# Kernel optimization log

Measured on AMD Instinct MI355X. Metric: run time of the kernel, lower is better.

The kernel has to match this reference:

```python
import jax, jax.numpy as jnp
import numpy as np

C = 512        # in_ch = n_heads * d_embed
NH = 8         # heads
DH = C // NH   # head dim = 64
G = 32         # groups
EPS_GN = 1e-6
EPS_LN = 1e-5


def group_norm(x, gamma, beta):
    # x: (B, C, H, W)
    B, Cc, H, W = x.shape
    xg = x.reshape(B, G, Cc // G, H, W)
    mu = xg.mean(axis=(2, 3, 4), keepdims=True)
    var = xg.var(axis=(2, 3, 4), keepdims=True)
    xg = (xg - mu) * jax.lax.rsqrt(var + EPS_GN)
    x = xg.reshape(B, Cc, H, W)
    return x * gamma[None, :, None, None] + beta[None, :, None, None]


def layer_norm(x, gamma, beta):
    mu = x.mean(axis=-1, keepdims=True)
    var = x.var(axis=-1, keepdims=True)
    return (x - mu) * jax.lax.rsqrt(var + EPS_LN) * gamma + beta


def mhsa(x, w_qkv, w_out, b_out):
    # x: (B, S, C); w_qkv: (C, 3C); w_out: (C, C)
    B, S, Cc = x.shape
    qkv = x @ w_qkv                                   # (B, S, 3C)
    q, k, v = jnp.split(qkv, 3, axis=-1)
    q = q.reshape(B, S, NH, DH).transpose(0, 2, 1, 3)  # (B, H, S, D)
    k = k.reshape(B, S, NH, DH).transpose(0, 2, 1, 3)
    v = v.reshape(B, S, NH, DH).transpose(0, 2, 1, 3)
    scores = jnp.einsum('bhsd,bhtd->bhst', q, k) / jnp.sqrt(jnp.float32(DH))
    attn = jax.nn.softmax(scores, axis=-1)
    o = jnp.einsum('bhst,bhtd->bhsd', attn, v)         # (B, H, S, D)
    o = o.transpose(0, 2, 1, 3).reshape(B, S, Cc)
    return o @ w_out + b_out


def conv1x1(x, w, b):
    # x: (B, C, H, W); w: (Cout, Cin)
    return jnp.einsum('oc,bchw->bohw', w, x) + b[None, :, None, None]


def reference(x, gn_g, gn_b, w_cin, b_cin,
              ln1_g, ln1_b, qkv1, out1_w, out1_b,
              ln2_g, ln2_b, qkv2, out2_w, out2_b,
              ln3_g, ln3_b, g1_w, g1_b, g2_w, g2_b,
              w_cout, b_cout):
    residue_long = x
    h = group_norm(x, gn_g, gn_b)
    h = conv1x1(h, w_cin, b_cin)
    B, Cc, H, W = h.shape
    h = h.reshape(B, Cc, H * W).transpose(0, 2, 1)     # (B, S, C)

    r = h
    h = mhsa(layer_norm(h, ln1_g, ln1_b), qkv1, out1_w, out1_b) + r
    r = h
    h = mhsa(layer_norm(h, ln2_g, ln2_b), qkv2, out2_w, out2_b) + r
    r = h
    g = layer_norm(h, ln3_g, ln3_b) @ g1_w + g1_b      # (B, S, 8C)
    val, gate = jnp.split(g, 2, axis=-1)
    h = (val * jax.nn.gelu(gate, approximate=False)) @ g2_w + g2_b
    h = h + r

    h = h.transpose(0, 2, 1).reshape(B, Cc, H, W)
    return conv1x1(h, w_cout, b_cout) + residue_long


def setup_inputs() -> dict:
    key = jax.random.key(0)
    ks = jax.random.split(key, 16)
    s = lambda n: 1.0 / np.sqrt(n)
    return {
        'x': jax.random.normal(ks[0], (8, C, 32, 32), jnp.float32),
        'gn_g': jnp.ones((C,), jnp.float32),
        'gn_b': jnp.zeros((C,), jnp.float32),
        'w_cin': jax.random.normal(ks[1], (C, C), jnp.float32) * s(C),
        'b_cin': jnp.zeros((C,), jnp.float32),
        'ln1_g': jnp.ones((C,), jnp.float32),
        'ln1_b': jnp.zeros((C,), jnp.float32),
        'qkv1': jax.random.normal(ks[2], (C, 3 * C), jnp.float32) * s(C),
        'out1_w': jax.random.normal(ks[3], (C, C), jnp.float32) * s(C),
        'out1_b': jnp.zeros((C,), jnp.float32),
        'ln2_g': jnp.ones((C,), jnp.float32),
        'ln2_b': jnp.zeros((C,), jnp.float32),
        'qkv2': jax.random.normal(ks[4], (C, 3 * C), jnp.float32) * s(C),
        'out2_w': jax.random.normal(ks[5], (C, C), jnp.float32) * s(C),
        'out2_b': jnp.zeros((C,), jnp.float32),
        'ln3_g': jnp.ones((C,), jnp.float32),
        'ln3_b': jnp.zeros((C,), jnp.float32),
        'g1_w': jax.random.normal(ks[6], (C, 8 * C), jnp.float32) * s(C),
        'g1_b': jnp.zeros((8 * C,), jnp.float32),
        'g2_w': jax.random.normal(ks[7], (4 * C, C), jnp.float32) * s(4 * C),
        'g2_b': jnp.zeros((C,), jnp.float32),
        'w_cout': jax.random.normal(ks[8], (C, C), jnp.float32) * s(C),
        'b_cout': jnp.zeros((C,), jnp.float32),
    }
```

## Files before the change

### kernel.cpp

```cpp
#include <hip/hip_runtime.h>
#include <hip/hip_bf16.h>
#include <math.h>

typedef __hip_bfloat16 bf16;

typedef __bf16 bf16x8 __attribute__((ext_vector_type(8)));
typedef float f32x4 __attribute__((ext_vector_type(4)));
typedef short shortx8 __attribute__((ext_vector_type(8)));

__device__ __forceinline__ float b2f_us(unsigned short u) {
    unsigned int v = ((unsigned int)u) << 16;
    return __builtin_bit_cast(float, v);
}
__device__ __forceinline__ unsigned short f2b_us(float f) {
    return __builtin_bit_cast(unsigned short, __float2bfloat16(f));
}
__device__ __forceinline__ float4 ld4(const float* p) { return *(const float4*)p; }
__device__ __forceinline__ float4 ld4(const bf16* p) {
    ushort4 u = *(const ushort4*)p;
    return make_float4(b2f_us(u.x), b2f_us(u.y), b2f_us(u.z), b2f_us(u.w));
}
__device__ __forceinline__ bf16x8 ldfrag(const bf16* p) {
    return __builtin_bit_cast(bf16x8, *(const shortx8*)p);
}
__device__ __forceinline__ f32x4 mfma16(bf16x8 a, bf16x8 b, f32x4 c) {
    return __builtin_amdgcn_mfma_f32_16x16x32_bf16(a, b, c, 0, 0, 0);
}
__device__ __forceinline__ void gload16(const bf16* g, bf16* l) {
    __builtin_amdgcn_global_load_lds(
        (const __attribute__((address_space(1))) void*)g,
        (__attribute__((address_space(3))) void*)l, 16, 0, 0);
}

struct WJob { const float* src; bf16* dst; int R, C, tile0, trans; };
struct WJobs { WJob j[8]; };

__global__ __launch_bounds__(256) void wconv_all(WJobs jobs) {
    __shared__ float tl[32][33];
    int bid = blockIdx.x;
    int ji = 0;
#pragma unroll
    for (int i = 1; i < 8; ++i)
        if (bid >= jobs.j[i].tile0) ji = i;
    WJob jb = jobs.j[ji];
    int t = bid - jb.tile0;
    int tc = jb.C >> 5;
    int tr_ = t / tc, tcx = t - tr_ * tc;
    int r0 = tr_ * 32, c0 = tcx * 32;
    const int tx = threadIdx.x & 31, ty = threadIdx.x >> 5;
    if (jb.trans) {
#pragma unroll
        for (int i = 0; i < 4; ++i)
            tl[ty + i * 8][tx] = jb.src[(long)(r0 + ty + i * 8) * jb.C + c0 + tx];
        __syncthreads();
#pragma unroll
        for (int i = 0; i < 4; ++i)
            jb.dst[(long)(c0 + ty + i * 8) * jb.R + r0 + tx] =
                __float2bfloat16(tl[tx][ty + i * 8]);
    } else {
#pragma unroll
        for (int i = 0; i < 4; ++i) {
            long idx = (long)(r0 + ty + i * 8) * jb.C + c0 + tx;
            jb.dst[idx] = __float2bfloat16(jb.src[idx]);
        }
    }
}

__global__ __launch_bounds__(256) void gn_stats_k(const float* __restrict__ x,
                                                  float* __restrict__ stats) {
    int bg = blockIdx.x;
    long base = (long)bg * 16384;
    int tid = threadIdx.x;
    float s = 0.f, sq = 0.f;
    for (int it = 0; it < 16; ++it) {
        float4 v = *(const float4*)(x + base + (long)it * 1024 + tid * 4);
        s += v.x + v.y + v.z + v.w;
        sq += v.x * v.x + v.y * v.y + v.z * v.z + v.w * v.w;
    }
#pragma unroll
    for (int off = 32; off; off >>= 1) {
        s += __shfl_down(s, off);
        sq += __shfl_down(sq, off);
    }
    __shared__ float r0[4], r1[4];
    if ((tid & 63) == 0) { r0[tid >> 6] = s; r1[tid >> 6] = sq; }
    __syncthreads();
    if (tid == 0) {
        s = r0[0] + r0[1] + r0[2] + r0[3];
        sq = r1[0] + r1[1] + r1[2] + r1[3];
        float mu = s * (1.f / 16384.f);
        float var = sq * (1.f / 16384.f) - mu * mu;
        stats[bg] = mu;
        stats[256 + bg] = rsqrtf(var + 1e-6f);
    }
}

__global__ __launch_bounds__(256) void gnxt_k(const float* __restrict__ x,
                                              const float* __restrict__ stats,
                                              const float* __restrict__ gng,
                                              const float* __restrict__ gnb,
                                              bf16* __restrict__ xt) {
    const int b = blockIdx.z;
    const int c0 = blockIdx.y * 64, s0 = blockIdx.x * 64;
    __shared__ float t[64][65];
    const int tx = threadIdx.x & 15, ty = threadIdx.x >> 4;
#pragma unroll
    for (int i = 0; i < 4; ++i) {
        int c = c0 + ty + i * 16;
        float rs = stats[256 + b * 32 + (c >> 4)];
        float ga = gng[c] * rs;
        float be = gnb[c] - stats[b * 32 + (c >> 4)] * ga;
        float4 v = *(const float4*)(x + ((long)b * 512 + c) * 1024 + s0 + tx * 4);
        t[ty + i * 16][tx * 4 + 0] = v.x * ga + be;
        t[ty + i * 16][tx * 4 + 1] = v.y * ga + be;
        t[ty + i * 16][tx * 4 + 2] = v.z * ga + be;
        t[ty + i * 16][tx * 4 + 3] = v.w * ga + be;
    }
    __syncthreads();
#pragma unroll
    for (int i = 0; i < 4; ++i) {
        int s = s0 + ty + i * 16;
        ushort4 o;
        o.x = f2b_us(t[tx * 4 + 0][ty + i * 16]);
        o.y = f2b_us(t[tx * 4 + 1][ty + i * 16]);
        o.z = f2b_us(t[tx * 4 + 2][ty + i * 16]);
        o.w = f2b_us(t[tx * 4 + 3][ty + i * 16]);
        *(ushort4*)(xt + ((long)b * 1024 + s) * 512 + c0 + tx * 4) = o;
    }
}

__global__ __launch_bounds__(256) void ln_k(const bf16* __restrict__ in,
                                            const float* __restrict__ g,
                                            const float* __restrict__ bvec,
                                            bf16* __restrict__ out) {
    long row = blockIdx.x;
    const bf16* p = in + row * 512;
    int tid = threadIdx.x;
    float v0 = b2f_us(__builtin_bit_cast(unsigned short, p[tid]));
    float v1 = b2f_us(__builtin_bit_cast(unsigned short, p[tid + 256]));
    float s = v0 + v1, sq = v0 * v0 + v1 * v1;
#pragma unroll
    for (int off = 32; off; off >>= 1) {
        s += __shfl_down(s, off);
        sq += __shfl_down(sq, off);
    }
    __shared__ float r0[4], r1[4];
    if ((tid & 63) == 0) { r0[tid >> 6] = s; r1[tid >> 6] = sq; }
    __syncthreads();
    s = r0[0] + r0[1] + r0[2] + r0[3];
    sq = r1[0] + r1[1] + r1[2] + r1[3];
    float mu = s * (1.f / 512.f);
    float var = sq * (1.f / 512.f) - mu * mu;
    float rs = rsqrtf(var + 1e-5f);
    out[row * 512 + tid] = __float2bfloat16((v0 - mu) * rs * g[tid] + bvec[tid]);
    out[row * 512 + tid + 256] =
        __float2bfloat16((v1 - mu) * rs * g[tid + 256] + bvec[tid + 256]);
}

template <bool HASBIAS, bool HASRES, bool VSPLIT>
__global__ __launch_bounds__(512, 4) void mm256_k(
    const bf16* __restrict__ A, const bf16* __restrict__ Bw,
    const float* __restrict__ bias, const bf16* __restrict__ res,
    bf16* __restrict__ C, bf16* __restrict__ vtout,
    int lda, int ldb, int ldc, int NT) {
    __shared__ bf16 sA[16384];
    __shared__ bf16 sB[8192];
    const int lane = threadIdx.x & 63, wave = threadIdx.x >> 6;
    const int lr = lane & 15, lg = lane >> 4;
    const int wm = wave >> 1, wn = wave & 1;
    const int m0 = blockIdx.x * 256, n0 = blockIdx.y * 128;

    f32x4 acc[4][4];
#pragma unroll
    for (int i = 0; i < 4; ++i)
#pragma unroll
        for (int j = 0; j < 4; ++j) acc[i][j] = (f32x4){0.f, 0.f, 0.f, 0.f};

    for (int t = 0; t < NT; ++t) {
        const int k0 = t * 64;
#pragma unroll
        for (int q = 0; q < 4; ++q) {
            int st = wave * 4 + q;
            int kh = st >> 4, sm = st & 15;
            gload16(A + (long)(m0 + sm * 16 + lr) * lda + k0 + kh * 32 + lg * 8,
                    &sA[st << 9]);
        }
#pragma unroll
        for (int q = 0; q < 2; ++q) {
            int bs = wave * 2 + q;
            int kh = bs >> 3, sn = bs & 7;
            gload16(Bw + (long)(n0 + sn * 16 + lr) * ldb + k0 + kh * 32 + lg * 8,
                    &sB[bs << 9]);
        }
        asm volatile("s_waitcnt vmcnt(0) lgkmcnt(0)" ::: "memory");
        __builtin_amdgcn_s_barrier();
#pragma unroll
        for (int kh = 0; kh < 2; ++kh) {
            bf16x8 af[4], bfr[4];
#pragma unroll
            for (int i = 0; i < 4; ++i)
                af[i] = ldfrag(&sA[((kh * 16 + wm * 4 + i) << 9) + lane * 8]);
#pragma unroll
            for (int j = 0; j < 4; ++j)
                bfr[j] = ldfrag(&sB[((kh * 8 + wn * 4 + j) << 9) + lane * 8]);
#pragma unroll
            for (int i = 0; i < 4; ++i)
#pragma unroll
                for (int j = 0; j < 4; ++j)
                    acc[i][j] = mfma16(af[i], bfr[j], acc[i][j]);
        }
        __builtin_amdgcn_s_barrier();
    }

    if (VSPLIT && n0 >= 1024) {
#pragma unroll
        for (int i = 0; i < 4; ++i) {
            int row = m0 + wm * 64 + i * 16 + lg * 4;
            int bb = row >> 10, ss = row & 1023;
#pragma unroll
            for (int j = 0; j < 4; ++j) {
                int col = n0 + wn * 64 + j * 16 + lr;
                int v = col - 1024;
                int hh = v >> 6, dd = v & 63;
                ushort4 o4;
                o4.x = f2b_us(acc[i][j][0]);
                o4.y = f2b_us(acc[i][j][1]);
                o4.z = f2b_us(acc[i][j][2]);
                o4.w = f2b_us(acc[i][j][3]);
                *(ushort4*)(vtout + ((long)(bb * 8 + hh) * 64 + dd) * 1024 + ss) = o4;
            }
        }
        return;
    }
#pragma unroll
    for (int i = 0; i < 4; ++i) {
        int row = m0 + wm * 64 + i * 16 + lg * 4;
#pragma unroll
        for (int j = 0; j < 4; ++j) {
            int col = n0 + wn * 64 + j * 16 + lr;
            float bv = HASBIAS ? bias[col] : 0.f;
#pragma unroll
            for (int r = 0; r < 4; ++r) {
                float v = acc[i][j][r] + bv;
                if (HASRES)
                    v += b2f_us(__builtin_bit_cast(unsigned short,
                             res[(long)(row + r) * ldc + col]));
                C[(long)(row + r) * ldc + col] = __float2bfloat16(v);
            }
        }
    }
}

__global__ __launch_bounds__(512, 4) void mm256_geglu_k(
    const bf16* __restrict__ A, const bf16* __restrict__ Bv,
    const bf16* __restrict__ Bg, const float* __restrict__ bias,
    bf16* __restrict__ C, int NT) {
    __shared__ bf16 sA[16384];
    __shared__ bf16 sB[8192];
    const int lane = threadIdx.x & 63, wave = threadIdx.x >> 6;
    const int lr = lane & 15, lg = lane >> 4;
    const int wm = wave >> 1, wn = wave & 1;
    const int m0 = blockIdx.x * 256, n0 = blockIdx.y * 64;

    f32x4 accv[4][2], accg[4][2];
#pragma unroll
    for (int i = 0; i < 4; ++i)
#pragma unroll
        for (int j = 0; j < 2; ++j) {
            accv[i][j] = (f32x4){0.f, 0.f, 0.f, 0.f};
            accg[i][j] = (f32x4){0.f, 0.f, 0.f, 0.f};
        }

    for (int t = 0; t < NT; ++t) {
        const int k0 = t * 64;
#pragma unroll
        for (int q = 0; q < 4; ++q) {
            int st = wave * 4 + q;
            int kh = st >> 4, sm = st & 15;
            gload16(A + (long)(m0 + sm * 16 + lr) * 512 + k0 + kh * 32 + lg * 8,
                    &sA[st << 9]);
        }
#pragma unroll
        for (int q = 0; q < 2; ++q) {
            int f = wave * 2 + q;
            int kh = f >> 3, r = f & 7;
            const bf16* bsrc = (r < 4) ? Bv : Bg;
            int sn = r & 3;
            gload16(bsrc + (long)(n0 + sn * 16 + lr) * 512 + k0 + kh * 32 + lg * 8,
                    &sB[f << 9]);
        }
        asm volatile("s_waitcnt vmcnt(0) lgkmcnt(0)" ::: "memory");
        __builtin_amdgcn_s_barrier();
#pragma unroll
        for (int kh = 0; kh < 2; ++kh) {
            bf16x8 af[4], bv_[2], bg_[2];
#pragma unroll
            for (int i = 0; i < 4; ++i)
                af[i] = ldfrag(&sA[((kh * 16 + wm * 4 + i) << 9) + lane * 8]);
#pragma unroll
            for (int j = 0; j < 2; ++j) {
                bv_[j] = ldfrag(&sB[((kh * 8 + wn * 2 + j) << 9) + lane * 8]);
                bg_[j] = ldfrag(&sB[((kh * 8 + 4 + wn * 2 + j) << 9) + lane * 8]);
            }
#pragma unroll
            for (int i = 0; i < 4; ++i)
#pragma unroll
                for (int j = 0; j < 2; ++j) {
                    accv[i][j] = mfma16(af[i], bv_[j], accv[i][j]);
                    accg[i][j] = mfma16(af[i], bg_[j], accg[i][j]);
                }
        }
        __builtin_amdgcn_s_barrier();
    }

#pragma unroll
    for (int i = 0; i < 4; ++i) {
        int row = m0 + wm * 64 + i * 16 + lg * 4;
#pragma unroll
        for (int j = 0; j < 2; ++j) {
            int col = n0 + (wn * 2 + j) * 16 + lr;
            float bv = bias[col], bg2 = bias[2048 + col];
#pragma unroll
            for (int r = 0; r < 4; ++r) {
                float v = accv[i][j][r] + bv;
                float g = accg[i][j][r] + bg2;
                float gl = 0.5f * g * (1.f + erff(g * 0.70710678118654752f));
                C[(long)(row + r) * 2048 + col] = __float2bfloat16(v * gl);
            }
        }
    }
}

template <bool HASBIAS, bool HASRES, int BN>
__global__ __launch_bounds__(256, 3) void mm_k(
    const bf16* __restrict__ A, const bf16* __restrict__ Bw,
    const float* __restrict__ bias, const bf16* __restrict__ res,
    bf16* __restrict__ C, int lda, int ldb, int ldc, int NT) {
    constexpr int NJ = BN / 64 * 2;
    __shared__ bf16 sA[8192];
    __shared__ bf16 sB[BN == 128 ? 8192 : 4096];
    const int lane = threadIdx.x & 63, wave = threadIdx.x >> 6;
    const int lr = lane & 15, lg = lane >> 4;
    const int wm = wave >> 1, wn = wave & 1;
    const int m0 = blockIdx.y * 128, n0 = blockIdx.x * BN;

    f32x4 acc[4][NJ];
#pragma unroll
    for (int i = 0; i < 4; ++i)
#pragma unroll
        for (int j = 0; j < NJ; ++j) acc[i][j] = (f32x4){0.f, 0.f, 0.f, 0.f};

    for (int t = 0; t < NT; ++t) {
        const int k0 = t * 64;
#pragma unroll
        for (int q = 0; q < 4; ++q) {
            int st = wave * 4 + q;
            int kh = st >> 3, sm = st & 7;
            gload16(A + (long)(m0 + sm * 16 + lr) * lda + k0 + kh * 32 + lg * 8,
                    &sA[st << 9]);
        }
        if (BN == 128) {
#pragma unroll
            for (int q = 0; q < 4; ++q) {
                int st = wave * 4 + q;
                int kh = st >> 3, sn = st & 7;
                gload16(Bw + (long)(n0 + sn * 16 + lr) * ldb + k0 + kh * 32 + lg * 8,
                        &sB[st << 9]);
            }
        } else {
#pragma unroll
            for (int q = 0; q < 2; ++q) {
                int bs = wave * 2 + q;
                int kh = bs >> 2, sn = bs & 3;
                gload16(Bw + (long)(n0 + sn * 16 + lr) * ldb + k0 + kh * 32 + lg * 8,
                        &sB[bs << 9]);
            }
        }
        asm volatile("s_waitcnt vmcnt(0) lgkmcnt(0)" ::: "memory");
        __builtin_amdgcn_s_barrier();
#pragma unroll
        for (int kh = 0; kh < 2; ++kh) {
            bf16x8 af[4], bfr[NJ];
#pragma unroll
            for (int i = 0; i < 4; ++i)
                af[i] = ldfrag(&sA[((kh * 8 + wm * 4 + i) << 9) + lane * 8]);
#pragma unroll
            for (int j = 0; j < NJ; ++j) {
                int bs = BN == 128 ? (kh * 8 + wn * 4 + j) : (kh * 4 + wn * 2 + j);
                bfr[j] = ldfrag(&sB[(bs << 9) + lane * 8]);
            }
#pragma unroll
            for (int i = 0; i < 4; ++i)
#pragma unroll
                for (int j = 0; j < NJ; ++j)
                    acc[i][j] = mfma16(af[i], bfr[j], acc[i][j]);
        }
        __builtin_amdgcn_s_barrier();
    }

#pragma unroll
    for (int i = 0; i < 4; ++i) {
        int row = m0 + wm * 64 + i * 16 + lg * 4;
#pragma unroll
        for (int j = 0; j < NJ; ++j) {
            int col = n0 + wn * (BN / 2) + j * 16 + lr;
            float bv = HASBIAS ? bias[col] : 0.f;
#pragma unroll
            for (int r = 0; r < 4; ++r) {
                float v = acc[i][j][r] + bv;
                if (HASRES)
                    v += b2f_us(__builtin_bit_cast(unsigned short,
                             res[(long)(row + r) * ldc + col]));
                C[(long)(row + r) * ldc + col] = __float2bfloat16(v);
            }
        }
    }
}

__global__ __launch_bounds__(256) void attn_mfma_k(const bf16* __restrict__ qkv,
                                                   const bf16* __restrict__ vt,
                                                   bf16* __restrict__ o) {
    const int wave = threadIdx.x >> 6, lane = threadIdx.x & 63;
    const int lr = lane & 15, lg = lane >> 4;
    const int h = blockIdx.y, b = blockIdx.z;
    const int q0 = blockIdx.x * 128 + wave * 32;
    __shared__ bf16 sKV[16384];
    __shared__ bf16 plds[4][16][72];
    bf16* pl = &plds[wave][0][0];
    const bf16* qbase = qkv + (long)b * 1024 * 1536 + h * 64;
    const bf16* kbase = qbase + 512;
    const bf16* vbase = vt + ((long)(b * 8 + h) * 64) * 1024;

    bf16x8 qf[2][2];
#pragma unroll
    for (int s = 0; s < 2; ++s) {
        const bf16* qp = qbase + (long)(q0 + s * 16 + lr) * 1536 + lg * 8;
#pragma unroll
        for (int c = 0; c < 2; ++c) {
            shortx8 raw = *(const shortx8*)(qp + c * 32);
            shortx8 sc;
#pragma unroll
            for (int j = 0; j < 8; ++j)
                sc[j] = __builtin_bit_cast(short,
                    f2b_us(b2f_us((unsigned short)raw[j]) * 0.125f));
            qf[s][c] = __builtin_bit_cast(bf16x8, sc);
        }
    }

    f32x4 of[2][4];
    float mrow[2][4], lrow[2][4];
#pragma unroll
    for (int s = 0; s < 2; ++s)
#pragma unroll
        for (int r = 0; r < 4; ++r) {
            of[s][r] = (f32x4){0.f, 0.f, 0.f, 0.f};
            mrow[s][r] = -1e30f;
            lrow[s][r] = 0.f;
        }

    auto computeKV = [&](const bf16* base) {
        f32x4 sf[2][4];
        __builtin_amdgcn_s_setprio(1);
#pragma unroll
        for (int kt = 0; kt < 4; ++kt) {
            bf16x8 k0f = ldfrag(base + (kt * 2) * 512 + lane * 8);
            bf16x8 k1f = ldfrag(base + (kt * 2 + 1) * 512 + lane * 8);
#pragma unroll
            for (int s = 0; s < 2; ++s) {
                f32x4 z = {0.f, 0.f, 0.f, 0.f};
                z = mfma16(qf[s][0], k0f, z);
                z = mfma16(qf[s][1], k1f, z);
                sf[s][kt] = z;
            }
        }
        __builtin_amdgcn_s_setprio(0);

        bf16x8 pa[2][2];
#pragma unroll
        for (int s = 0; s < 2; ++s) {
            float mt[4];
#pragma unroll
            for (int r = 0; r < 4; ++r)
                mt[r] = fmaxf(fmaxf(sf[s][0][r], sf[s][1][r]),
                              fmaxf(sf[s][2][r], sf[s][3][r]));
#pragma unroll
            for (int m = 1; m < 16; m <<= 1)
#pragma unroll
                for (int r = 0; r < 4; ++r)
                    mt[r] = fmaxf(mt[r], __shfl_xor(mt[r], m));
            float need = mt[0] - mrow[s][0];
#pragma unroll
            for (int r = 1; r < 4; ++r) need = fmaxf(need, mt[r] - mrow[s][r]);
            if (!__all(need <= 8.f)) {
#pragma unroll
                for (int r = 0; r < 4; ++r) {
                    float mn = fmaxf(mrow[s][r], mt[r]);
                    float al = __expf(mrow[s][r] - mn);
                    mrow[s][r] = mn;
                    lrow[s][r] *= al;
#pragma unroll
                    for (int dt = 0; dt < 4; ++dt) of[s][dt][r] *= al;
                }
            }
            float psum[4] = {0.f, 0.f, 0.f, 0.f};
#pragma unroll
            for (int kt = 0; kt < 4; ++kt)
#pragma unroll
                for (int r = 0; r < 4; ++r) {
                    float p = __expf(sf[s][kt][r] - mrow[s][r]);
                    psum[r] += p;
                    pl[(lg * 4 + r) * 72 + kt * 16 + lr] = __float2bfloat16(p);
                }
#pragma unroll
            for (int m = 1; m < 16; m <<= 1)
#pragma unroll
                for (int r = 0; r < 4; ++r)
                    psum[r] += __shfl_xor(psum[r], m);
#pragma unroll
            for (int r = 0; r < 4; ++r) lrow[s][r] += psum[r];
            pa[s][0] = ldfrag(pl + lr * 72 + lg * 8);
            pa[s][1] = ldfrag(pl + lr * 72 + 32 + lg * 8);
        }
        __builtin_amdgcn_s_setprio(1);
#pragma unroll
        for (int dt = 0; dt < 4; ++dt) {
            bf16x8 v0f = ldfrag(base + (8 + dt * 2) * 512 + lane * 8);
            bf16x8 v1f = ldfrag(base + (8 + dt * 2 + 1) * 512 + lane * 8);
#pragma unroll
            for (int s = 0; s < 2; ++s) {
                of[s][dt] = mfma16(pa[s][0], v0f, of[s][dt]);
                of[s][dt] = mfma16(pa[s][1], v1f, of[s][dt]);
            }
        }
        __builtin_amdgcn_s_setprio(0);
    };

    for (int t = 0; t < 8; ++t) {
        const int kv0 = t * 128;
#pragma unroll
        for (int q = 0; q < 8; ++q) {
            int st = wave * 8 + q;
            int chunk = st >> 4, r = st & 15;
            int kvb = kv0 + chunk * 64;
            const bf16* src;
            if (r < 8)
                src = kbase + (long)(kvb + (r >> 1) * 16 + lr) * 1536 +
                      (r & 1) * 32 + lg * 8;
            else {
                int vs = r - 8;
                src = vbase + (long)((vs >> 1) * 16 + lr) * 1024 + kvb +
                      (vs & 1) * 32 + lg * 8;
            }
            gload16(src, &sKV[st << 9]);
        }
        asm volatile("s_waitcnt vmcnt(0) lgkmcnt(0)" ::: "memory");
        __builtin_amdgcn_s_barrier();
        computeKV(&sKV[0]);
        computeKV(&sKV[8192]);
        __builtin_amdgcn_s_barrier();
    }

#pragma unroll
    for (int s = 0; s < 2; ++s) {
        bf16* op = o + ((long)b * 1024 + q0 + s * 16 + lg * 4) * 512 + h * 64 + lr;
#pragma unroll
        for (int r = 0; r < 4; ++r) {
            float inv = 1.f / lrow[s][r];
#pragma unroll
            for (int dt = 0; dt < 4; ++dt)
                op[(long)r * 512 + dt * 16] = __float2bfloat16(of[s][dt][r] * inv);
        }
    }
}

__global__ __launch_bounds__(256) void outepi_k(const bf16* __restrict__ tmp,
                                                const float* __restrict__ bcout,
                                                const float* __restrict__ x,
                                                float* __restrict__ out) {
    const int b = blockIdx.z;
    const int o0 = blockIdx.y * 64, s0 = blockIdx.x * 64;
    __shared__ float t[64][65];
    const int tx = threadIdx.x & 15, ty = threadIdx.x >> 4;
#pragma unroll
    for (int i = 0; i < 4; ++i) {
        int s = s0 + ty + i * 16;
        float4 v = ld4(tmp + ((long)b * 1024 + s) * 512 + o0 + tx * 4);
        t[ty + i * 16][tx * 4 + 0] = v.x;
        t[ty + i * 16][tx * 4 + 1] = v.y;
        t[ty + i * 16][tx * 4 + 2] = v.z;
        t[ty + i * 16][tx * 4 + 3] = v.w;
    }
    __syncthreads();
#pragma unroll
    for (int i = 0; i < 4; ++i) {
        int o = o0 + ty + i * 16;
        long idx = ((long)b * 512 + o) * 1024 + s0 + tx * 4;
        float4 xr = *(const float4*)(x + idx);
        float bc = bcout[o];
        float4 w;
        w.x = t[tx * 4 + 0][ty + i * 16] + bc + xr.x;
        w.y = t[tx * 4 + 1][ty + i * 16] + bc + xr.y;
        w.z = t[tx * 4 + 2][ty + i * 16] + bc + xr.z;
        w.w = t[tx * 4 + 3][ty + i * 16] + bc + xr.w;
        *(float4*)(out + idx) = w;
    }
}

extern "C" void kernel_launch(void* const* d_in, const int* in_sizes, int n_in,
                              void* d_out, int out_size, void* d_ws, size_t ws_size,
                              hipStream_t stream) {
    const float* x = (const float*)d_in[0];
    const float* gn_g = (const float*)d_in[1];
    const float* gn_b = (const float*)d_in[2];
    const float* w_cin = (const float*)d_in[3];
    const float* b_cin = (const float*)d_in[4];
    const float* ln1_g = (const float*)d_in[5];
    const float* ln1_b = (const float*)d_in[6];
    const float* qkv1w = (const float*)d_in[7];
    const float* out1_w = (const float*)d_in[8];
    const float* out1_b = (const float*)d_in[9];
    const float* ln2_g = (const float*)d_in[10];
    const float* ln2_b = (const float*)d_in[11];
    const float* qkv2w = (const float*)d_in[12];
    const float* out2_w = (const float*)d_in[13];
    const float* out2_b = (const float*)d_in[14];
    const float* ln3_g = (const float*)d_in[15];
    const float* ln3_b = (const float*)d_in[16];
    const float* g1_w = (const float*)d_in[17];
    const float* g1_b = (const float*)d_in[18];
    const float* g2_w = (const float*)d_in[19];
    const float* g2_b = (const float*)d_in[20];
    const float* w_cout = (const float*)d_in[21];
    const float* b_cout = (const float*)d_in[22];
    float* out = (float*)d_out;

    char* ws = (char*)d_ws;
    float* stats = (float*)ws;
    bf16* wq1 = (bf16*)(ws + 4096);
    bf16* wo1 = wq1 + 1536 * 512;
    bf16* wq2 = wo1 + 512 * 512;
    bf16* wo2 = wq2 + 1536 * 512;
    bf16* wg1 = wo2 + 512 * 512;
    bf16* wg2 = wg1 + 4096 * 512;
    bf16* wci = wg2 + 512 * 2048;
    bf16* wco = wci + 512 * 512;
    bf16* h = wco + 512 * 512;
    bf16* h2 = h + (size_t)8192 * 512;
    bf16* lnb = h2 + (size_t)8192 * 512;
    bf16* qkv = lnb + (size_t)8192 * 512;
    bf16* obuf = qkv + (size_t)8192 * 1536;
    bf16* gg = qkv;
    bf16* vt = obuf;

    WJobs jobs;
    jobs.j[0] = {qkv1w, wq1, 512, 1536, 0, 1};
    jobs.j[1] = {out1_w, wo1, 512, 512, 768, 1};
    jobs.j[2] = {qkv2w, wq2, 512, 1536, 1024, 1};
    jobs.j[3] = {out2_w, wo2, 512, 512, 1792, 1};
    jobs.j[4] = {g1_w, wg1, 512, 4096, 2048, 1};
    jobs.j[5] = {g2_w, wg2, 2048, 512, 4096, 1};
    jobs.j[6] = {w_cin, wci, 512, 512, 5120, 0};
    jobs.j[7] = {w_cout, wco, 512, 512, 5376, 0};
    wconv_all<<<5632, 256, 0, stream>>>(jobs);

    gn_stats_k<<<256, 256, 0, stream>>>(x, stats);
    gnxt_k<<<dim3(16, 8, 8), 256, 0, stream>>>(x, stats, gn_g, gn_b, lnb);
    mm_k<true, false, 64><<<dim3(8, 64), 256, 0, stream>>>(
        lnb, wci, b_cin, nullptr, h, 512, 512, 512, 8);

    ln_k<<<8192, 256, 0, stream>>>(h, ln1_g, ln1_b, lnb);
    mm256_k<false, false, true><<<dim3(32, 12), 512, 0, stream>>>(
        lnb, wq1, nullptr, nullptr, qkv, vt, 512, 512, 1536, 8);
    attn_mfma_k<<<dim3(8, 8, 8), 256, 0, stream>>>(qkv, vt, lnb);
    mm_k<true, true, 64><<<dim3(8, 64), 256, 0, stream>>>(
        lnb, wo1, out1_b, h, h2, 512, 512, 512, 8);

    ln_k<<<8192, 256, 0, stream>>>(h2, ln2_g, ln2_b, lnb);
    mm256_k<false, false, true><<<dim3(32, 12), 512, 0, stream>>>(
        lnb, wq2, nullptr, nullptr, qkv, vt, 512, 512, 1536, 8);
    attn_mfma_k<<<dim3(8, 8, 8), 256, 0, stream>>>(qkv, vt, lnb);
    mm_k<true, true, 64><<<dim3(8, 64), 256, 0, stream>>>(
        lnb, wo2, out2_b, h2, h, 512, 512, 512, 8);

    ln_k<<<8192, 256, 0, stream>>>(h, ln3_g, ln3_b, lnb);
    mm256_geglu_k<<<dim3(32, 32), 512, 0, stream>>>(
        lnb, wg1, wg1 + (size_t)2048 * 512, g1_b, gg, 8);
    mm_k<true, true, 64><<<dim3(8, 64), 256, 0, stream>>>(
        gg, wg2, g2_b, h, h2, 2048, 2048, 512, 32);

    mm_k<false, false, 64><<<dim3(8, 64), 256, 0, stream>>>(
        h2, wco, nullptr, nullptr, lnb, 512, 512, 512, 8);
    outepi_k<<<dim3(16, 8, 8), 256, 0, stream>>>(lnb, b_cout, x, out);
}
```

Measured before the change: 401.4 us.

## Triple-buffer GEGLU GEMM LDS with interleaved prefetch and MFMA priority

Rewrites the GEGLU projection GEMM to use a three-slot shared-memory ring, prefetching K tiles two iterations ahead and spreading the global loads between MFMA sub-steps. Partial vmcnt waits replace the full drain, and s_setprio raises priority during MFMA bursts. This targets load latency that was previously exposed each K iteration. In exchange, LDS use roughly triples, occupancy drops to one block per CU, and more barriers are added.

```diff
diff --git a/kernel.cpp b/kernel.cpp
--- a/kernel.cpp
+++ b/kernel.cpp
@@ -251,12 +251,12 @@
     }
 }
 
-__global__ __launch_bounds__(512, 4) void mm256_geglu_k(
+__global__ __launch_bounds__(512, 1) void mm8p_geglu_k(
     const bf16* __restrict__ A, const bf16* __restrict__ Bv,
     const bf16* __restrict__ Bg, const float* __restrict__ bias,
     bf16* __restrict__ C, int NT) {
-    __shared__ bf16 sA[16384];
-    __shared__ bf16 sB[8192];
+    __shared__ bf16 sA[3][16384];
+    __shared__ bf16 sB[3][8192];
     const int lane = threadIdx.x & 63, wave = threadIdx.x >> 6;
     const int lr = lane & 15, lg = lane >> 4;
     const int wm = wave >> 1, wn = wave & 1;
@@ -271,15 +271,15 @@
             accg[i][j] = (f32x4){0.f, 0.f, 0.f, 0.f};
         }
 
-    for (int t = 0; t < NT; ++t) {
-        const int k0 = t * 64;
-#pragma unroll
-        for (int q = 0; q < 4; ++q) {
-            int st = wave * 4 + q;
-            int kh = st >> 4, sm = st & 15;
+    auto stageA = [&](int slot, int k0, int kh) {
+#pragma unroll
+        for (int q = 0; q < 2; ++q) {
+            int sm = wave * 2 + q;
             gload16(A + (long)(m0 + sm * 16 + lr) * 512 + k0 + kh * 32 + lg * 8,
-                    &sA[st << 9]);
-        }
+                    &sA[slot][(kh * 16 + sm) << 9]);
+        }
+    };
+    auto stageB = [&](int slot, int k0) {
 #pragma unroll
         for (int q = 0; q < 2; ++q) {
             int f = wave * 2 + q;
@@ -287,30 +287,59 @@
             const bf16* bsrc = (r < 4) ? Bv : Bg;
             int sn = r & 3;
             gload16(bsrc + (long)(n0 + sn * 16 + lr) * 512 + k0 + kh * 32 + lg * 8,
-                    &sB[f << 9]);
-        }
-        asm volatile("s_waitcnt vmcnt(0) lgkmcnt(0)" ::: "memory");
+                    &sB[slot][f << 9]);
+        }
+    };
+
+    stageA(0, 0, 0); stageA(0, 0, 1); stageB(0, 0);
+    stageA(1, 64, 0); stageA(1, 64, 1); stageB(1, 64);
+
+    for (int t = 0; t < NT; ++t) {
+        const int slot = t % 3;
+        const int s2 = (t + 2) % 3;
+        const int k2 = (t + 2) * 64;
+        const bool more = (t + 2) < NT;
+        if (t + 1 < NT)
+            asm volatile("s_waitcnt vmcnt(6)" ::: "memory");
+        else
+            asm volatile("s_waitcnt vmcnt(0)" ::: "memory");
         __builtin_amdgcn_s_barrier();
-#pragma unroll
-        for (int kh = 0; kh < 2; ++kh) {
-            bf16x8 af[4], bv_[2], bg_[2];
-#pragma unroll
-            for (int i = 0; i < 4; ++i)
-                af[i] = ldfrag(&sA[((kh * 16 + wm * 4 + i) << 9) + lane * 8]);
-#pragma unroll
-            for (int j = 0; j < 2; ++j) {
-                bv_[j] = ldfrag(&sB[((kh * 8 + wn * 2 + j) << 9) + lane * 8]);
-                bg_[j] = ldfrag(&sB[((kh * 8 + 4 + wn * 2 + j) << 9) + lane * 8]);
-            }
-#pragma unroll
-            for (int i = 0; i < 4; ++i)
+
+        bf16x8 bv_[2][2], bg_[2][2];
+#pragma unroll
+        for (int mi = 0; mi < 4; ++mi) {
+            bf16x8 a0 = ldfrag(&sA[slot][((wm * 4 + mi) << 9) + lane * 8]);
+            bf16x8 a1 = ldfrag(&sA[slot][((16 + wm * 4 + mi) << 9) + lane * 8]);
+            if (mi == 0) {
+#pragma unroll
+                for (int kh = 0; kh < 2; ++kh)
+#pragma unroll
+                    for (int j = 0; j < 2; ++j) {
+                        bv_[kh][j] = ldfrag(
+                            &sB[slot][((kh * 8 + wn * 2 + j) << 9) + lane * 8]);
+                        bg_[kh][j] = ldfrag(
+                            &sB[slot][((kh * 8 + 4 + wn * 2 + j) << 9) + lane * 8]);
+                    }
+            }
+            if (more) {
+                if (mi == 0) stageA(s2, k2, 0);
+                if (mi == 1) stageA(s2, k2, 1);
+                if (mi == 2) stageB(s2, k2);
+            }
+            __builtin_amdgcn_s_barrier();
+            __builtin_amdgcn_s_setprio(1);
+#pragma unroll
+            for (int kh = 0; kh < 2; ++kh) {
+                bf16x8 a = kh ? a1 : a0;
 #pragma unroll
                 for (int j = 0; j < 2; ++j) {
-                    accv[i][j] = mfma16(af[i], bv_[j], accv[i][j]);
-                    accg[i][j] = mfma16(af[i], bg_[j], accg[i][j]);
+                    accv[mi][j] = mfma16(a, bv_[kh][j], accv[mi][j]);
+                    accg[mi][j] = mfma16(a, bg_[kh][j], accg[mi][j]);
                 }
-        }
-        __builtin_amdgcn_s_barrier();
+            }
+            __builtin_amdgcn_s_setprio(0);
+            if (mi < 3) __builtin_amdgcn_s_barrier();
+        }
     }
 
 #pragma unroll
@@ -683,7 +712,7 @@
         lnb, wo2, out2_b, h2, h, 512, 512, 512, 8);
 
     ln_k<<<8192, 256, 0, stream>>>(h, ln3_g, ln3_b, lnb);
-    mm256_geglu_k<<<dim3(32, 32), 512, 0, stream>>>(
+    mm8p_geglu_k<<<dim3(32, 32), 512, 0, stream>>>(
         lnb, wg1, wg1 + (size_t)2048 * 512, g1_b, gg, 8);
     mm_k<true, true, 64><<<dim3(8, 64), 256, 0, stream>>>(
         gg, wg2, g2_b, h, h2, 2048, 2048, 512, 32);
```

Result: slower. 414.8 us (+3.3%).
